# Kernel tuning notes

Hardware: AMD Instinct MI355X
Metric: run time of the kernel (lower is better)

## Reference

```python
import jax, jax.numpy as jnp
import numpy as np

N_NODES = 50000
N_EDGES = 800000
IN_CH = 128
HEADS = 4
OUT_CH = 4
N_GRAPHS = 64
NEG_SLOPE = 0.2  # GATv2Conv default leaky_relu slope
EPS = 1e-5       # GraphNorm eps


def _seg_sum(x, seg, n):
    return jax.ops.segment_sum(x, seg, num_segments=n)


def _seg_mean(x, seg, n):
    s = _seg_sum(x, seg, n)
    cnt = _seg_sum(jnp.ones((seg.shape[0],), x.dtype), seg, n)
    return s / jnp.maximum(cnt, 1.0)[:, None]


def gatv2_conv(x, src, dst, n, w_l, w_r, att, bias, heads, out_ch, concat):
    # x: [N, F_in]; src/dst: [E_tot] (self-loops already appended)
    x_l = (x @ w_l).reshape(n, heads, out_ch)
    x_r = (x @ w_r).reshape(n, heads, out_ch)
    m = jax.nn.leaky_relu(x_l[src] + x_r[dst], NEG_SLOPE)   # [E, H, C]
    e = jnp.einsum('ehc,hc->eh', m, att)                    # [E, H]
    # softmax over incoming edges of each destination node
    e_max = jax.ops.segment_max(e, dst, num_segments=n)     # [N, H]
    w = jnp.exp(e - e_max[dst])
    denom = _seg_sum(w, dst, n)                             # [N, H]
    alpha = w / denom[dst]
    out = _seg_sum(alpha[:, :, None] * x_l[src], dst, n)    # [N, H, C]
    out = out.reshape(n, heads * out_ch) if concat else out.mean(axis=1)
    return out + bias


def graph_norm(x, batch, weight, bias, mean_scale, n_graphs):
    mu = _seg_mean(x, batch, n_graphs)                      # [G, C]
    out = x - mu[batch] * mean_scale
    var = _seg_mean(out * out, batch, n_graphs)
    return out / jnp.sqrt(var[batch] + EPS) * weight + bias


def setup_inputs() -> dict:
    key = jax.random.key(0)
    ks = jax.random.split(key, 20)
    H = HEADS
    d = {}
    d['x'] = jax.random.normal(ks[0], (N_NODES, IN_CH), dtype=jnp.float32)
    d['edge_index'] = jax.random.randint(ks[1], (2, N_EDGES), 0, N_NODES, dtype=jnp.int32)
    d['batch'] = jnp.sort(jax.random.randint(ks[2], (N_NODES,), 0, N_GRAPHS, dtype=jnp.int32))
    def glorot(k, shape):
        fan = shape[0] + shape[-1]
        return jax.random.normal(k, shape, dtype=jnp.float32) * np.sqrt(2.0 / fan).astype(np.float32)
    # layer 1: in 128 -> 32 per head, concat -> 128
    d['w_l1'] = glorot(ks[3], (IN_CH, H * 32)); d['w_r1'] = glorot(ks[4], (IN_CH, H * 32))
    d['att1'] = glorot(ks[5], (H, 32)); d['b1'] = jnp.zeros((H * 32,), jnp.float32)
    d['gn1_w'] = jnp.ones((H * 32,), jnp.float32); d['gn1_b'] = jnp.zeros((H * 32,), jnp.float32); d['gn1_s'] = jnp.ones((H * 32,), jnp.float32)
    # layer 2: 128 -> 16 per head, concat -> 64
    d['w_l2'] = glorot(ks[6], (H * 32, H * 16)); d['w_r2'] = glorot(ks[7], (H * 32, H * 16))
    d['att2'] = glorot(ks[8], (H, 16)); d['b2'] = jnp.zeros((H * 16,), jnp.float32)
    d['gn2_w'] = jnp.ones((H * 16,), jnp.float32); d['gn2_b'] = jnp.zeros((H * 16,), jnp.float32); d['gn2_s'] = jnp.ones((H * 16,), jnp.float32)
    # layer 3: 64 -> 8 per head, mean over heads -> 8
    d['w_l3'] = glorot(ks[9], (H * 16, H * 8)); d['w_r3'] = glorot(ks[10], (H * 16, H * 8))
    d['att3'] = glorot(ks[11], (H, 8)); d['b3'] = jnp.zeros((8,), jnp.float32)
    d['gn3_w'] = jnp.ones((8,), jnp.float32); d['gn3_b'] = jnp.zeros((8,), jnp.float32); d['gn3_s'] = jnp.ones((8,), jnp.float32)
    d['lin_w'] = glorot(ks[12], (8, OUT_CH)); d['lin_b'] = jnp.zeros((OUT_CH,), jnp.float32)
    return d


def reference(x, edge_index, batch,
              w_l1, w_r1, att1, b1, gn1_w, gn1_b, gn1_s,
              w_l2, w_r2, att2, b2, gn2_w, gn2_b, gn2_s,
              w_l3, w_r3, att3, b3, gn3_w, gn3_b, gn3_s,
              lin_w, lin_b):
    n = x.shape[0]
    loop = jnp.arange(n, dtype=edge_index.dtype)
    src = jnp.concatenate([edge_index[0], loop])  # add_self_loops=True (PyG default)
    dst = jnp.concatenate([edge_index[1], loop])
    h = gatv2_conv(x, src, dst, n, w_l1, w_r1, att1, b1, HEADS, 32, True)
    h = jax.nn.relu(graph_norm(h, batch, gn1_w, gn1_b, gn1_s, N_GRAPHS))
    h = gatv2_conv(h, src, dst, n, w_l2, w_r2, att2, b2, HEADS, 16, True)
    h = jax.nn.relu(graph_norm(h, batch, gn2_w, gn2_b, gn2_s, N_GRAPHS))
    h = gatv2_conv(h, src, dst, n, w_l3, w_r3, att3, b3, HEADS, 8, False)
    h = jax.nn.relu(graph_norm(h, batch, gn3_w, gn3_b, gn3_s, N_GRAPHS))
    features = _seg_mean(h, batch, N_GRAPHS)  # global_mean_pool -> [G, 8]
    logits = features @ lin_w + lin_b         # [G, OUT_CH]
    return (logits, features)
```

## Files before the change

kernel.cpp:

```cpp
#include <hip/hip_runtime.h>
#include <hip/hip_fp16.h>
#include <math.h>

#define NN 50000
#define NE 800000
#define ET (NE + NN)
#define NG 64
#define H 4
#define NBK 196
#define CH 2048
#define SB ((ET + CH - 1) / CH)
#define GD ((NN + 63) / 64)

typedef _Float16 half8 __attribute__((ext_vector_type(8)));
typedef _Float16 half4 __attribute__((ext_vector_type(4)));
typedef _Float16 hv2 __attribute__((ext_vector_type(2)));
typedef float floatx4 __attribute__((ext_vector_type(4)));


template <int K, int M2>
__device__ __forceinline__ void wprep_fn(int chunk, const float* __restrict__ Wl, const float* __restrict__ Wr,
                                         _Float16* __restrict__ Wfrag) {
    constexpr int MTOT = 2 * M2, NT = MTOT / 16;
    if (chunk >= MTOT * K / 8) return;
    int lane = chunk & 63, tt = chunk >> 6;
    int t = tt % NT, kt = tt / NT;
    int n = t * 16 + (lane & 15);
    int kb = kt * 32 + (lane >> 4) * 8;
    const float* src = (n < M2) ? (Wl + n) : (Wr + (n - M2));
    half8 h;
#pragma unroll
    for (int j = 0; j < 8; ++j) h[j] = (_Float16)src[(size_t)(kb + j) * M2];
    *(half8*)(Wfrag + (size_t)chunk * 8) = h;
}


__global__ __launch_bounds__(256) void k_prep(const float* __restrict__ Wl1, const float* __restrict__ Wr1,
                                              const float* __restrict__ Wl2, const float* __restrict__ Wr2,
                                              const float* __restrict__ Wl3, const float* __restrict__ Wr3,
                                              _Float16* __restrict__ Wf1, _Float16* __restrict__ Wf2,
                                              _Float16* __restrict__ Wf3,
                                              const int* __restrict__ batch, int* __restrict__ bpos,
                                              const int* __restrict__ ei, int* __restrict__ bcnt) {
    int b = blockIdx.x, t = threadIdx.x;
    if (b < 16) { wprep_fn<128, 128>(b * 256 + t, Wl1, Wr1, Wf1); return; }
    if (b < 24) { wprep_fn<128, 64>((b - 16) * 256 + t, Wl2, Wr2, Wf2); return; }
    if (b < 26) { wprep_fn<64, 32>((b - 24) * 256 + t, Wl3, Wr3, Wf3); return; }
    if (b < 26 + NBK) {
        int i = (b - 26) * 256 + t;
        if (i >= NN) return;
        int cur = batch[i];
        int prev = (i == 0) ? -1 : batch[i - 1];
        for (int g = prev + 1; g <= cur; ++g) bpos[g] = i;
        if (i == NN - 1)
            for (int g = cur + 1; g <= NG; ++g) bpos[g] = NN;
        return;
    }
    __shared__ int hist[NBK];
    int b0 = b - 26 - NBK;
    for (int i = t; i < NBK; i += 256) hist[i] = 0;
    __syncthreads();
#pragma unroll
    for (int pass = 0; pass < CH / 256; ++pass) {
        int e = b0 * CH + pass * 256 + t;
        if (e < ET) {
            int d = (e < NE) ? ei[NE + e] : (e - NE);
            atomicAdd(&hist[d >> 8], 1);
        }
    }
    __syncthreads();
    if (t < NBK) bcnt[t * SB + b0] = hist[t];
}


template <typename AT, bool NORM>
__device__ __forceinline__ half8 load_a8(const AT* __restrict__ ap, const float* __restrict__ pa,
                                         const float* __restrict__ pb) {
    if constexpr (NORM) {
        half8 raw = *(const half8*)ap;
        half8 h;
#pragma unroll
        for (int j = 0; j < 8; ++j) {
            float y = fmaf((float)raw[j], pa[j], pb[j]);
            h[j] = (_Float16)fmaxf(y, 0.f);
        }
        return h;
    } else if constexpr (__is_same(AT, _Float16)) {
        return *(const half8*)ap;
    } else {
        const float4* p = (const float4*)ap;
        float4 a = p[0], b = p[1];
        half8 h;
        h[0] = (_Float16)a.x; h[1] = (_Float16)a.y; h[2] = (_Float16)a.z; h[3] = (_Float16)a.w;
        h[4] = (_Float16)b.x; h[5] = (_Float16)b.y; h[6] = (_Float16)b.z; h[7] = (_Float16)b.w;
        return h;
    }
}

template <int K, int M2, typename AT, bool NORM>
__device__ __forceinline__ void dualgemm_body(int blk, int tid, const AT* __restrict__ Ain,
                                              const _Float16* __restrict__ Wfrag,
                                              __half* __restrict__ Ol, float* __restrict__ Or,
                                              const float* __restrict__ ga, const float* __restrict__ gb,
                                              const int* __restrict__ batch) {
    constexpr int MTOT = 2 * M2;
    constexpr int NT = MTOT / 16;
    constexpr int KT = K / 32;
    int wid = tid >> 6, lane = tid & 63;
    int q = lane >> 4, l15 = lane & 15;
    int r0 = blk * 64 + wid * 16;
    int arow = min(r0 + l15, NN - 1);
    const AT* ap = Ain + (size_t)arow * K + q * 8;
    const float *pa = nullptr, *pb = nullptr;
    if constexpr (NORM) {
        int g = batch[arow];
        pa = ga + g * K + q * 8;
        pb = gb + g * K + q * 8;
    }

    floatx4 acc[NT];
#pragma unroll
    for (int t = 0; t < NT; ++t) acc[t] = (floatx4){0.f, 0.f, 0.f, 0.f};

#pragma unroll
    for (int kt = 0; kt < KT; ++kt) {
        half8 a8 = load_a8<AT, NORM>(ap + kt * 32, pa + (NORM ? kt * 32 : 0), pb + (NORM ? kt * 32 : 0));
        const _Float16* wp = Wfrag + ((size_t)(kt * NT) * 64 + lane) * 8;
#pragma unroll
        for (int t = 0; t < NT; ++t) {
            half8 b8 = *(const half8*)(wp + (size_t)t * 64 * 8);
            acc[t] = __builtin_amdgcn_mfma_f32_16x16x32_f16(a8, b8, acc[t], 0, 0, 0);
        }
    }

#pragma unroll
    for (int t = 0; t < NT; ++t) {
        int cn = t * 16 + l15;
#pragma unroll
        for (int reg = 0; reg < 4; ++reg) {
            int r = r0 + q * 4 + reg;
            if (r < NN) {
                if (cn < M2) Ol[(size_t)r * M2 + cn] = __float2half(acc[t][reg]);
                else         Or[(size_t)r * M2 + (cn - M2)] = acc[t][reg];
            }
        }
    }
}

template <int K, int M2>
__global__ __launch_bounds__(256) void k_dualgemm_n(const __half* __restrict__ Ain,
                                                    const _Float16* __restrict__ Wfrag,
                                                    __half* __restrict__ Ol, float* __restrict__ Or,
                                                    const float* __restrict__ ga, const float* __restrict__ gb,
                                                    const int* __restrict__ batch) {
    dualgemm_body<K, M2, _Float16, true>(blockIdx.x, threadIdx.x, (const _Float16*)Ain, Wfrag, Ol, Or,
                                         ga, gb, batch);
}


__device__ __forceinline__ void bscanA_fn(int b, int t, const int* __restrict__ bcnt,
                                          int* __restrict__ boff, int* __restrict__ tot) {
    __shared__ int lds[256];
    int i0 = 2 * t, i1 = 2 * t + 1;
    int v0 = (i0 < SB) ? bcnt[b * SB + i0] : 0;
    int v1 = (i1 < SB) ? bcnt[b * SB + i1] : 0;
    int pair = v0 + v1;
    lds[t] = pair;
    __syncthreads();
    for (int off = 1; off < 256; off <<= 1) {
        int y = (t >= off) ? lds[t - off] : 0;
        __syncthreads();
        lds[t] += y;
        __syncthreads();
    }
    int excl = lds[t] - pair;
    if (i0 < SB) boff[b * SB + i0] = excl;
    if (i1 < SB) boff[b * SB + i1] = excl + v0;
    if (t == 255) tot[b] = lds[255];
}


__global__ __launch_bounds__(256) void k_gemm1_scan(const float* __restrict__ x, const _Float16* __restrict__ Wf1,
                                                    __half* __restrict__ Ol, float* __restrict__ Or,
                                                    const int* __restrict__ bcnt, int* __restrict__ boff,
                                                    int* __restrict__ tot) {
    if (blockIdx.x < GD)
        dualgemm_body<128, 128, float, false>(blockIdx.x, threadIdx.x, x, Wf1, Ol, Or, nullptr, nullptr, nullptr);
    else
        bscanA_fn(blockIdx.x - GD, threadIdx.x, bcnt, boff, tot);
}


__device__ __forceinline__ void edge_sd(int e, const int* __restrict__ ei, int& s, int& d) {
    if (e < NE) { s = ei[e]; d = ei[NE + e]; } else { s = e - NE; d = s; }
}

__global__ __launch_bounds__(256) void k_bscatter(const int* __restrict__ ei, const int* __restrict__ tot,
                                                  const int* __restrict__ boff, unsigned int* __restrict__ ebuf) {
    __shared__ int eb[256];
    __shared__ int cur[NBK];
    int b0 = blockIdx.x, t = threadIdx.x;
    int v = (t < NBK) ? tot[t] : 0;
    eb[t] = v;
    __syncthreads();
    for (int off = 1; off < 256; off <<= 1) {
        int y = (t >= off) ? eb[t - off] : 0;
        __syncthreads();
        eb[t] += y;
        __syncthreads();
    }
    if (t < NBK) cur[t] = (eb[t] - v) + boff[t * SB + b0];
    __syncthreads();
#pragma unroll
    for (int pass = 0; pass < CH / 256; ++pass) {
        int e = b0 * CH + pass * 256 + t;
        if (e < ET) {
            int s, d;
            edge_sd(e, ei, s, d);
            int pos = atomicAdd(&cur[d >> 8], 1);
            ebuf[pos] = ((unsigned)s << 16) | (unsigned)(d & 255);
        }
    }
}


__global__ __launch_bounds__(256) void k_bsort(const unsigned int* __restrict__ ebuf,
                                               const int* __restrict__ tot,
                                               int* __restrict__ rowptr, unsigned short* __restrict__ colsrc) {
    __shared__ int eb[256];
    __shared__ int sbase;
    __shared__ int cnt2[256];
    __shared__ int sc[256];
    __shared__ int cur2[256];
    int b = blockIdx.x, t = threadIdx.x;
    int v = (t < NBK) ? tot[t] : 0;
    eb[t] = v;
    __syncthreads();
    for (int off = 1; off < 256; off <<= 1) {
        int y = (t >= off) ? eb[t - off] : 0;
        __syncthreads();
        eb[t] += y;
        __syncthreads();
    }
    if (t == b) sbase = eb[t] - v;
    __syncthreads();
    int base = sbase, n = tot[b];
    cnt2[t] = 0;
    __syncthreads();
    for (int i = t; i < n; i += 256) atomicAdd(&cnt2[ebuf[base + i] & 255], 1);
    __syncthreads();
    int cv = cnt2[t];
    sc[t] = cv;
    __syncthreads();
    for (int off = 1; off < 256; off <<= 1) {
        int y = (t >= off) ? sc[t - off] : 0;
        __syncthreads();
        sc[t] += y;
        __syncthreads();
    }
    int excl = sc[t] - cv;
    int d = b * 256 + t;
    if (d < NN) rowptr[d] = base + excl;
    if (b == 0 && t == 0) rowptr[NN] = ET;
    cur2[t] = excl;
    __syncthreads();
    for (int i = t; i < n; i += 256) {
        unsigned u = ebuf[base + i];
        int pos = atomicAdd(&cur2[u & 255], 1);
        colsrc[base + pos] = (unsigned short)(u >> 16);
    }
}


template <int CP> struct HVec { hv2 h2[CP / 2]; };

template <int CP>
__device__ __forceinline__ HVec<CP> load_hv(const __half* __restrict__ p) {
    HVec<CP> r;
    if constexpr (CP == 16) {
        float4* rp = (float4*)&r;
        rp[0] = ((const float4*)p)[0];
        rp[1] = ((const float4*)p)[1];
    } else if constexpr (CP == 8) {
        float4 t = *(const float4*)p; r = *(HVec<CP>*)&t;
    } else if constexpr (CP == 4) {
        float2 t = *(const float2*)p; r = *(HVec<CP>*)&t;
    } else {
        r.h2[0] = *(const hv2*)p;
    }
    return r;
}

template <int C, int EP, bool CONCAT>
__global__ __launch_bounds__(256) void k_attn(const __half* __restrict__ xl, const float* __restrict__ xr,
                                              const int* __restrict__ rowptr,
                                              const unsigned short* __restrict__ colsrc,
                                              const float* __restrict__ att, const float* __restrict__ bias,
                                              __half* __restrict__ out) {
    constexpr int CP = C / EP;
    constexpr int LEP = (EP == 4) ? 2 : ((EP == 2) ? 1 : 0);
    int t = blockIdx.x * 256 + threadIdx.x;
    int part = t & (EP - 1);
    int nh = t >> LEP;
    if (nh >= NN * H) return;
    int node = nh >> 2, h = nh & 3;
    int cbase = h * C + part * CP;
    hv2 xrr2[CP / 2], attv2[CP / 2];
    float acc[CP];
    {
        const float* p = xr + (size_t)node * (H * C) + cbase;
        const float* q = att + cbase;
#pragma unroll
        for (int j = 0; j < CP / 2; ++j) {
            xrr2[j] = (hv2){(_Float16)p[2 * j], (_Float16)p[2 * j + 1]};
            attv2[j] = (hv2){(_Float16)q[2 * j], (_Float16)q[2 * j + 1]};
        }
#pragma unroll
        for (int c = 0; c < CP; ++c) acc[c] = 0.f;
    }
    float denom = 0.f;
    int beg = rowptr[node], end = rowptr[node + 1];

    auto process = [&](const HVec<CP>& xv) {
        float part_s = 0.f;
#pragma unroll
        for (int j = 0; j < CP / 2; ++j) {
            hv2 z = xv.h2[j] + xrr2[j];
            hv2 l = __builtin_elementwise_max(z, z * (_Float16)0.2f);
            part_s = __builtin_amdgcn_fdot2(l, attv2[j], part_s, false);
        }
        float score = part_s;
#pragma unroll
        for (int mask = 1; mask < EP; mask <<= 1) score += __shfl_xor(score, mask, 64);
        float w = __expf(score);
        denom += w;
        const _Float16* xh = (const _Float16*)&xv;
#pragma unroll
        for (int c = 0; c < CP; ++c) acc[c] = fmaf(w, (float)xh[c], acc[c]);
    };

    int idx = beg;
    for (; idx + 4 <= end; idx += 4) {
        int s0 = colsrc[idx], s1 = colsrc[idx + 1], s2 = colsrc[idx + 2], s3 = colsrc[idx + 3];
        HVec<CP> xv0 = load_hv<CP>(xl + (size_t)s0 * (H * C) + cbase);
        HVec<CP> xv1 = load_hv<CP>(xl + (size_t)s1 * (H * C) + cbase);
        HVec<CP> xv2 = load_hv<CP>(xl + (size_t)s2 * (H * C) + cbase);
        HVec<CP> xv3 = load_hv<CP>(xl + (size_t)s3 * (H * C) + cbase);
        process(xv0);
        process(xv1);
        process(xv2);
        process(xv3);
    }
    for (; idx < end; ++idx) {
        int s = colsrc[idx];
        HVec<CP> xv = load_hv<CP>(xl + (size_t)s * (H * C) + cbase);
        process(xv);
    }

    float inv = 1.f / denom;
    _Float16* op = (_Float16*)out + (size_t)node * (H * C) + cbase;
    _Float16 hv[CP];
#pragma unroll
    for (int c = 0; c < CP; ++c) {
        float v = acc[c] * inv;
        if (CONCAT) v += bias[cbase + c];
        hv[c] = (_Float16)v;
    }
    if constexpr (CP >= 8) {
#pragma unroll
        for (int j = 0; j < CP / 8; ++j) *(half8*)(op + 8 * j) = *(half8*)(hv + 8 * j);
    } else if constexpr (CP == 4) {
        *(half4*)op = *(half4*)hv;
    } else {
        *(hv2*)op = *(hv2*)hv;
    }
}


template <int LOGC, int SPLIT>
__global__ __launch_bounds__(256) void k_gnred2(const __half* __restrict__ h, const int* __restrict__ bpos,
                                                float* __restrict__ sum, float* __restrict__ sumsq) {
    constexpr int C = 1 << LOGC;
    constexpr int RG = 256 >> LOGC;
    int g = blockIdx.x / SPLIT, s = blockIdx.x % SPLIT;
    int c = threadIdx.x & (C - 1);
    int rg = threadIdx.x >> LOGC;
    int b0 = bpos[g], b1 = bpos[g + 1];
    int n = b1 - b0;
    int seg = (n + SPLIT - 1) / SPLIT;
    int r0 = b0 + s * seg;
    int r1 = min(r0 + seg, b1);
    float sv = 0.f, ssv = 0.f;
    for (int r = r0 + rg; r < r1; r += RG) {
        float x = __half2float(h[(size_t)r * C + c]);
        sv += x; ssv += x * x;
    }
    __shared__ float ls[256], lss[256];
    ls[threadIdx.x] = sv; lss[threadIdx.x] = ssv;
    __syncthreads();
    for (int off = 128; off >= C; off >>= 1) {
        if (threadIdx.x < off) {
            ls[threadIdx.x] += ls[threadIdx.x + off];
            lss[threadIdx.x] += lss[threadIdx.x + off];
        }
        __syncthreads();
    }
    if (threadIdx.x < C) {
        atomicAdd(&sum[g * C + threadIdx.x], ls[threadIdx.x]);
        atomicAdd(&sumsq[g * C + threadIdx.x], lss[threadIdx.x]);
    }
}


__global__ __launch_bounds__(256) void k_gnparam(const float* __restrict__ sum, const float* __restrict__ sumsq,
                                                 const int* __restrict__ bpos, const float* __restrict__ w,
                                                 const float* __restrict__ b, const float* __restrict__ ms,
                                                 int logC, float* __restrict__ ga, float* __restrict__ gb) {
    int C = 1 << logC;
    int i = blockIdx.x * 256 + threadIdx.x;
    if (i >= NG * C) return;
    int g = i >> logC, c = i & (C - 1);
    float cg = fmaxf((float)(bpos[g + 1] - bpos[g]), 1.f);
    float mu = sum[i] / cg;
    float ex2 = sumsq[i] / cg;
    float s_ = ms[c];
    float var = ex2 - (2.f * s_ - s_ * s_) * mu * mu;
    float a = rsqrtf(var + 1e-5f) * w[c];
    ga[i] = a;
    gb[i] = b[c] - mu * s_ * a;
}


template <int SPLIT>
__global__ __launch_bounds__(256) void k_headgn(const __half* __restrict__ tmp, const float* __restrict__ b3,
                                                const int* __restrict__ bpos, float* __restrict__ Af,
                                                float* __restrict__ sum, float* __restrict__ sumsq) {
    constexpr int C = 8, RG = 32;
    int g = blockIdx.x / SPLIT, s = blockIdx.x % SPLIT;
    int c = threadIdx.x & 7;
    int rg = threadIdx.x >> 3;
    int b0 = bpos[g], b1 = bpos[g + 1];
    int n = b1 - b0;
    int seg = (n + SPLIT - 1) / SPLIT;
    int r0 = b0 + s * seg;
    int r1 = min(r0 + seg, b1);
    float bias = b3[c];
    float sv = 0.f, ssv = 0.f;
    for (int r = r0 + rg; r < r1; r += RG) {
        const __half* p = tmp + (size_t)r * 32 + c;
        float v = 0.25f * (__half2float(p[0]) + __half2float(p[8]) +
                           __half2float(p[16]) + __half2float(p[24])) + bias;
        Af[(size_t)r * C + c] = v;
        sv += v; ssv += v * v;
    }
    __shared__ float ls[256], lss[256];
    ls[threadIdx.x] = sv; lss[threadIdx.x] = ssv;
    __syncthreads();
    for (int off = 128; off >= C; off >>= 1) {
        if (threadIdx.x < off) {
            ls[threadIdx.x] += ls[threadIdx.x + off];
            lss[threadIdx.x] += lss[threadIdx.x + off];
        }
        __syncthreads();
    }
    if (threadIdx.x < C) {
        atomicAdd(&sum[g * C + threadIdx.x], ls[threadIdx.x]);
        atomicAdd(&sumsq[g * C + threadIdx.x], lss[threadIdx.x]);
    }
}

template <int SPLIT>
__global__ __launch_bounds__(256) void k_gnpool(const float* __restrict__ Af, const int* __restrict__ bpos,
                                                const float* __restrict__ sum, const float* __restrict__ sumsq,
                                                const float* __restrict__ w,
                                                const float* __restrict__ b, const float* __restrict__ ms,
                                                float* __restrict__ pool) {
    constexpr int C = 8, RG = 32;
    int g = blockIdx.x / SPLIT, s = blockIdx.x % SPLIT;
    int c = threadIdx.x & 7;
    int rg = threadIdx.x >> 3;
    int b0 = bpos[g], b1 = bpos[g + 1];
    int n = b1 - b0;
    int seg = (n + SPLIT - 1) / SPLIT;
    int r0 = b0 + s * seg;
    int r1 = min(r0 + seg, b1);
    float cg = fmaxf((float)n, 1.f);
    float mu = sum[g * C + c] / cg;
    float ex2 = sumsq[g * C + c] / cg;
    float s_ = ms[c];
    float var = ex2 - (2.f * s_ - s_ * s_) * mu * mu;
    float rs = rsqrtf(var + 1e-5f) * w[c];
    float bb = b[c], mus = mu * s_;
    float pv = 0.f;
    for (int r = r0 + rg; r < r1; r += RG) {
        float y = fmaxf((Af[(size_t)r * C + c] - mus) * rs + bb, 0.f);
        pv += y;
    }
    __shared__ float ls[256];
    ls[threadIdx.x] = pv;
    __syncthreads();
    for (int off = 128; off >= C; off >>= 1) {
        if (threadIdx.x < off) ls[threadIdx.x] += ls[threadIdx.x + off];
        __syncthreads();
    }
    if (threadIdx.x < C) atomicAdd(&pool[g * C + threadIdx.x], ls[threadIdx.x]);
}


__global__ __launch_bounds__(512) void k_final(const float* __restrict__ pool, const int* __restrict__ bpos,
                                               const float* __restrict__ lw, const float* __restrict__ lb,
                                               float* __restrict__ outp) {
    __shared__ float feat[512];
    int t = threadIdx.x;
    int g = t >> 3;
    float f = pool[t] / fmaxf((float)(bpos[g + 1] - bpos[g]), 1.f);
    feat[t] = f;
    outp[256 + t] = f;
    __syncthreads();
    if (t < 256) {
        int g2 = t >> 2, o = t & 3;
        float a = lb[o];
#pragma unroll
        for (int cc = 0; cc < 8; ++cc) a += feat[g2 * 8 + cc] * lw[cc * 4 + o];
        outp[t] = a;
    }
}


extern "C" void kernel_launch(void* const* d_in, const int* in_sizes, int n_in,
                              void* d_out, int out_size, void* d_ws, size_t ws_size,
                              hipStream_t stream) {
    const float* x    = (const float*)d_in[0];
    const int*   ei   = (const int*)d_in[1];
    const int*   batch= (const int*)d_in[2];
    const float *w_l1 = (const float*)d_in[3],  *w_r1 = (const float*)d_in[4];
    const float *att1 = (const float*)d_in[5],  *b1   = (const float*)d_in[6];
    const float *gn1w = (const float*)d_in[7],  *gn1b = (const float*)d_in[8],  *gn1s = (const float*)d_in[9];
    const float *w_l2 = (const float*)d_in[10], *w_r2 = (const float*)d_in[11];
    const float *att2 = (const float*)d_in[12], *b2   = (const float*)d_in[13];
    const float *gn2w = (const float*)d_in[14], *gn2b = (const float*)d_in[15], *gn2s = (const float*)d_in[16];
    const float *w_l3 = (const float*)d_in[17], *w_r3 = (const float*)d_in[18];
    const float *att3 = (const float*)d_in[19], *b3   = (const float*)d_in[20];
    const float *gn3w = (const float*)d_in[21], *gn3b = (const float*)d_in[22], *gn3s = (const float*)d_in[23];
    const float *lw   = (const float*)d_in[24], *lb   = (const float*)d_in[25];

    char* ws = (char*)d_ws;
    size_t off = 0;
    auto alloc = [&](size_t bytes) -> void* {
        void* p = ws + off;
        off += (bytes + 255) & ~(size_t)255;
        return p;
    };
    __half* Ah  = (__half*)alloc((size_t)NN * 128 * 2);
    __half* Bh  = (__half*)alloc((size_t)NN * 128 * 2);
    __half* Chh = (__half*)alloc((size_t)NN * 64 * 2);
    float*  B   = (float*)alloc((size_t)NN * 128 * 4);
    float*  Cb  = (float*)alloc((size_t)NN * 64 * 4);
    float*  Af  = (float*)alloc((size_t)NN * 8 * 4);
    _Float16* Wf1 = (_Float16*)alloc((size_t)256 * 128 * 2);
    _Float16* Wf2 = (_Float16*)alloc((size_t)128 * 128 * 2);
    _Float16* Wf3 = (_Float16*)alloc((size_t)64 * 64 * 2);
    float* ga1 = (float*)alloc((size_t)NG * 128 * 4);
    float* gb1 = (float*)alloc((size_t)NG * 128 * 4);
    float* ga2 = (float*)alloc((size_t)NG * 64 * 4);
    float* gb2 = (float*)alloc((size_t)NG * 64 * 4);
    int* rowptr = (int*)alloc((size_t)(NN + 1) * 4);
    unsigned short* colsrc = (unsigned short*)alloc((size_t)ET * 2);
    unsigned int* ebuf = (unsigned int*)alloc((size_t)ET * 4);
    int* bcnt   = (int*)alloc((size_t)NBK * SB * 4);
    int* boff   = (int*)alloc((size_t)NBK * SB * 4);
    int* tot    = (int*)alloc((size_t)NBK * 4);
    int* bpos   = (int*)alloc((size_t)(NG + 1) * 4);
    char* zbase = ws + off;
    float* sum1 = (float*)alloc((size_t)NG * 128 * 4);
    float* sq1  = (float*)alloc((size_t)NG * 128 * 4);
    float* sum2 = (float*)alloc((size_t)NG * 64 * 4);
    float* sq2  = (float*)alloc((size_t)NG * 64 * 4);
    float* sum3 = (float*)alloc((size_t)NG * 8 * 4);
    float* sq3  = (float*)alloc((size_t)NG * 8 * 4);
    float* pool = (float*)alloc((size_t)NG * 8 * 4);
    size_t zbytes = (size_t)((ws + off) - zbase);
    (void)hipMemsetAsync(zbase, 0, zbytes, stream);

    k_prep<<<26 + NBK + SB, 256, 0, stream>>>(w_l1, w_r1, w_l2, w_r2, w_l3, w_r3, Wf1, Wf2, Wf3,
                                              batch, bpos, ei, bcnt);
    k_gemm1_scan<<<GD + NBK, 256, 0, stream>>>(x, Wf1, Ah, B, bcnt, boff, tot);
    k_bscatter<<<SB, 256, 0, stream>>>(ei, tot, boff, ebuf);
    k_bsort<<<NBK, 256, 0, stream>>>(ebuf, tot, rowptr, colsrc);

    int gA2ep = (NN * H * 2 + 255) / 256;
    int gA1ep = (NN * H + 255) / 256;

    k_attn<32, 2, true><<<gA2ep, 256, 0, stream>>>(Ah, B, rowptr, colsrc, att1, b1, Bh);
    k_gnred2<7, 8><<<NG * 8, 256, 0, stream>>>(Bh, bpos, sum1, sq1);
    k_gnparam<<<(NG * 128 + 255) / 256, 256, 0, stream>>>(sum1, sq1, bpos, gn1w, gn1b, gn1s, 7, ga1, gb1);

    k_dualgemm_n<128, 64><<<GD, 256, 0, stream>>>(Bh, Wf2, Ah, Cb, ga1, gb1, batch);
    k_attn<16, 2, true><<<gA2ep, 256, 0, stream>>>(Ah, Cb, rowptr, colsrc, att2, b2, Chh);
    k_gnred2<6, 8><<<NG * 8, 256, 0, stream>>>(Chh, bpos, sum2, sq2);
    k_gnparam<<<(NG * 64 + 255) / 256, 256, 0, stream>>>(sum2, sq2, bpos, gn2w, gn2b, gn2s, 6, ga2, gb2);

    k_dualgemm_n<64, 32><<<GD, 256, 0, stream>>>(Chh, Wf3, Ah, B, ga2, gb2, batch);
    k_attn<8, 1, false><<<gA1ep, 256, 0, stream>>>(Ah, B, rowptr, colsrc, att3, nullptr, Bh);
    k_headgn<8><<<NG * 8, 256, 0, stream>>>(Bh, b3, bpos, Af, sum3, sq3);
    k_gnpool<8><<<NG * 8, 256, 0, stream>>>(Af, bpos, sum3, sq3, gn3w, gn3b, gn3s, pool);
    k_final<<<1, 512, 0, stream>>>(pool, bpos, lw, lb, (float*)d_out);
}
```

Measured before the change: 300.0 us.

## Fuse GraphNorm statistics into attention epilogue and norm params into next GEMM

The attention kernel now accumulates per-graph sum and sum-of-squares directly in its epilogue, using wave shuffles and a block reduction when all nodes in the block belong to one graph, and falls back to per-thread atomics otherwise. The separate gnred2, gnparam and headgn kernels are removed; the next dual GEMM computes the GraphNorm scale and shift on the fly from the raw sums. The right-side projection is also stored as fp16 instead of fp32. This cuts several launches and passes over the node features, at the cost of extra per-element math in the GEMM A-load, more atomics across graph boundaries, and fp16 rounding of x_r.

```diff
diff --git a/kernel.cpp b/kernel.cpp
--- a/kernel.cpp
+++ b/kernel.cpp
@@ -16,6 +16,15 @@
 typedef _Float16 half4 __attribute__((ext_vector_type(4)));
 typedef _Float16 hv2 __attribute__((ext_vector_type(2)));
 typedef float floatx4 __attribute__((ext_vector_type(4)));
+
+struct f8 { float v[8]; };
+__device__ __forceinline__ f8 ld8(const float* __restrict__ p) {
+    f8 r;
+    float4 a = ((const float4*)p)[0], b = ((const float4*)p)[1];
+    r.v[0] = a.x; r.v[1] = a.y; r.v[2] = a.z; r.v[3] = a.w;
+    r.v[4] = b.x; r.v[5] = b.y; r.v[6] = b.z; r.v[7] = b.w;
+    return r;
+}
 
 
 template <int K, int M2>
@@ -73,19 +82,9 @@
 }
 
 
-template <typename AT, bool NORM>
-__device__ __forceinline__ half8 load_a8(const AT* __restrict__ ap, const float* __restrict__ pa,
-                                         const float* __restrict__ pb) {
-    if constexpr (NORM) {
-        half8 raw = *(const half8*)ap;
-        half8 h;
-#pragma unroll
-        for (int j = 0; j < 8; ++j) {
-            float y = fmaf((float)raw[j], pa[j], pb[j]);
-            h[j] = (_Float16)fmaxf(y, 0.f);
-        }
-        return h;
-    } else if constexpr (__is_same(AT, _Float16)) {
+template <typename AT>
+__device__ __forceinline__ half8 load_raw8(const AT* __restrict__ ap) {
+    if constexpr (__is_same(AT, _Float16)) {
         return *(const half8*)ap;
     } else {
         const float4* p = (const float4*)ap;
@@ -100,9 +99,11 @@
 template <int K, int M2, typename AT, bool NORM>
 __device__ __forceinline__ void dualgemm_body(int blk, int tid, const AT* __restrict__ Ain,
                                               const _Float16* __restrict__ Wfrag,
-                                              __half* __restrict__ Ol, float* __restrict__ Or,
-                                              const float* __restrict__ ga, const float* __restrict__ gb,
-                                              const int* __restrict__ batch) {
+                                              __half* __restrict__ Ol, __half* __restrict__ Or,
+                                              const float* __restrict__ gsum, const float* __restrict__ gsq,
+                                              const float* __restrict__ gw, const float* __restrict__ gbb,
+                                              const float* __restrict__ gms,
+                                              const int* __restrict__ bpos, const int* __restrict__ batch) {
     constexpr int MTOT = 2 * M2;
     constexpr int NT = MTOT / 16;
     constexpr int KT = K / 32;
@@ -111,11 +112,11 @@
     int r0 = blk * 64 + wid * 16;
     int arow = min(r0 + l15, NN - 1);
     const AT* ap = Ain + (size_t)arow * K + q * 8;
-    const float *pa = nullptr, *pb = nullptr;
+    float inv_cg = 0.f;
+    int g = 0;
     if constexpr (NORM) {
-        int g = batch[arow];
-        pa = ga + g * K + q * 8;
-        pb = gb + g * K + q * 8;
+        g = batch[arow];
+        inv_cg = 1.f / fmaxf((float)(bpos[g + 1] - bpos[g]), 1.f);
     }
 
     floatx4 acc[NT];
@@ -124,7 +125,29 @@
 
 #pragma unroll
     for (int kt = 0; kt < KT; ++kt) {
-        half8 a8 = load_a8<AT, NORM>(ap + kt * 32, pa + (NORM ? kt * 32 : 0), pb + (NORM ? kt * 32 : 0));
+        half8 a8;
+        if constexpr (NORM) {
+            half8 raw = *(const half8*)(ap + kt * 32);
+            int c0 = kt * 32 + q * 8;
+            f8 su = ld8(gsum + (size_t)g * K + c0);
+            f8 sx = ld8(gsq + (size_t)g * K + c0);
+            f8 ww = ld8(gw + c0);
+            f8 bb = ld8(gbb + c0);
+            f8 mm = ld8(gms + c0);
+#pragma unroll
+            for (int j = 0; j < 8; ++j) {
+                float mu = su.v[j] * inv_cg;
+                float ex2 = sx.v[j] * inv_cg;
+                float s_ = mm.v[j];
+                float var = ex2 - s_ * (2.f - s_) * mu * mu;
+                float a = rsqrtf(var + 1e-5f) * ww.v[j];
+                float bsh = bb.v[j] - mu * s_ * a;
+                float y = fmaf((float)raw[j], a, bsh);
+                a8[j] = (_Float16)fmaxf(y, 0.f);
+            }
+        } else {
+            a8 = load_raw8<AT>(ap + kt * 32);
+        }
         const _Float16* wp = Wfrag + ((size_t)(kt * NT) * 64 + lane) * 8;
 #pragma unroll
         for (int t = 0; t < NT; ++t) {
@@ -141,7 +164,7 @@
             int r = r0 + q * 4 + reg;
             if (r < NN) {
                 if (cn < M2) Ol[(size_t)r * M2 + cn] = __float2half(acc[t][reg]);
-                else         Or[(size_t)r * M2 + (cn - M2)] = acc[t][reg];
+                else         Or[(size_t)r * M2 + (cn - M2)] = __float2half(acc[t][reg]);
             }
         }
     }
@@ -150,11 +173,13 @@
 template <int K, int M2>
 __global__ __launch_bounds__(256) void k_dualgemm_n(const __half* __restrict__ Ain,
                                                     const _Float16* __restrict__ Wfrag,
-                                                    __half* __restrict__ Ol, float* __restrict__ Or,
-                                                    const float* __restrict__ ga, const float* __restrict__ gb,
-                                                    const int* __restrict__ batch) {
+                                                    __half* __restrict__ Ol, __half* __restrict__ Or,
+                                                    const float* __restrict__ gsum, const float* __restrict__ gsq,
+                                                    const float* __restrict__ gw, const float* __restrict__ gbb,
+                                                    const float* __restrict__ gms,
+                                                    const int* __restrict__ bpos, const int* __restrict__ batch) {
     dualgemm_body<K, M2, _Float16, true>(blockIdx.x, threadIdx.x, (const _Float16*)Ain, Wfrag, Ol, Or,
-                                         ga, gb, batch);
+                                         gsum, gsq, gw, gbb, gms, bpos, batch);
 }
 
 
@@ -181,11 +206,12 @@
 
 
 __global__ __launch_bounds__(256) void k_gemm1_scan(const float* __restrict__ x, const _Float16* __restrict__ Wf1,
-                                                    __half* __restrict__ Ol, float* __restrict__ Or,
+                                                    __half* __restrict__ Ol, __half* __restrict__ Or,
                                                     const int* __restrict__ bcnt, int* __restrict__ boff,
                                                     int* __restrict__ tot) {
     if (blockIdx.x < GD)
-        dualgemm_body<128, 128, float, false>(blockIdx.x, threadIdx.x, x, Wf1, Ol, Or, nullptr, nullptr, nullptr);
+        dualgemm_body<128, 128, float, false>(blockIdx.x, threadIdx.x, x, Wf1, Ol, Or,
+                                              nullptr, nullptr, nullptr, nullptr, nullptr, nullptr, nullptr);
     else
         bscanA_fn(blockIdx.x - GD, threadIdx.x, bcnt, boff, tot);
 }
@@ -292,34 +318,41 @@
 }
 
 template <int C, int EP, bool CONCAT>
-__global__ __launch_bounds__(256) void k_attn(const __half* __restrict__ xl, const float* __restrict__ xr,
+__global__ __launch_bounds__(256) void k_attn(const __half* __restrict__ xl, const __half* __restrict__ xr,
                                               const int* __restrict__ rowptr,
                                               const unsigned short* __restrict__ colsrc,
                                               const float* __restrict__ att, const float* __restrict__ bias,
-                                              __half* __restrict__ out) {
+                                              __half* __restrict__ out,
+                                              const int* __restrict__ batch,
+                                              float* __restrict__ gsum, float* __restrict__ gsq,
+                                              float* __restrict__ Af) {
     constexpr int CP = C / EP;
     constexpr int LEP = (EP == 4) ? 2 : ((EP == 2) ? 1 : 0);
+    constexpr int TPN = H * EP;
+    constexpr int NPB = 256 / TPN;
     int t = blockIdx.x * 256 + threadIdx.x;
     int part = t & (EP - 1);
     int nh = t >> LEP;
-    if (nh >= NN * H) return;
-    int node = nh >> 2, h = nh & 3;
+    bool active = (nh < NN * H);
+    int node = active ? (nh >> 2) : (NN - 1);
+    int h = nh & 3;
     int cbase = h * C + part * CP;
     hv2 xrr2[CP / 2], attv2[CP / 2];
     float acc[CP];
     {
-        const float* p = xr + (size_t)node * (H * C) + cbase;
+        HVec<CP> xrv = load_hv<CP>(xr + (size_t)node * (H * C) + cbase);
         const float* q = att + cbase;
 #pragma unroll
         for (int j = 0; j < CP / 2; ++j) {
-            xrr2[j] = (hv2){(_Float16)p[2 * j], (_Float16)p[2 * j + 1]};
+            xrr2[j] = xrv.h2[j];
             attv2[j] = (hv2){(_Float16)q[2 * j], (_Float16)q[2 * j + 1]};
         }
 #pragma unroll
         for (int c = 0; c < CP; ++c) acc[c] = 0.f;
     }
     float denom = 0.f;
-    int beg = rowptr[node], end = rowptr[node + 1];
+    int beg = active ? rowptr[node] : 0;
+    int end = active ? rowptr[node + 1] : 0;
 
     auto process = [&](const HVec<CP>& xv) {
         float part_s = 0.f;
@@ -358,116 +391,118 @@
     }
 
     float inv = 1.f / denom;
-    _Float16* op = (_Float16*)out + (size_t)node * (H * C) + cbase;
-    _Float16 hv[CP];
-#pragma unroll
-    for (int c = 0; c < CP; ++c) {
-        float v = acc[c] * inv;
-        if (CONCAT) v += bias[cbase + c];
-        hv[c] = (_Float16)v;
-    }
-    if constexpr (CP >= 8) {
-#pragma unroll
-        for (int j = 0; j < CP / 8; ++j) *(half8*)(op + 8 * j) = *(half8*)(hv + 8 * j);
-    } else if constexpr (CP == 4) {
-        *(half4*)op = *(half4*)hv;
+    int node0 = blockIdx.x * NPB;
+    int nodeL = min(node0 + NPB, NN) - 1;
+    int gf = batch[node0], gl = batch[nodeL];
+    int lane = threadIdx.x & 63, wv = threadIdx.x >> 6;
+
+    if constexpr (CONCAT) {
+#pragma unroll
+        for (int c = 0; c < CP; ++c) {
+            float v = acc[c] * inv + bias[cbase + c];
+            acc[c] = active ? v : 0.f;
+        }
+        if (active) {
+            _Float16* op = (_Float16*)out + (size_t)node * (H * C) + cbase;
+            _Float16 hv[CP];
+#pragma unroll
+            for (int c = 0; c < CP; ++c) hv[c] = (_Float16)acc[c];
+            if constexpr (CP >= 8) {
+#pragma unroll
+                for (int j = 0; j < CP / 8; ++j) *(half8*)(op + 8 * j) = *(half8*)(hv + 8 * j);
+            } else if constexpr (CP == 4) {
+                *(half4*)op = *(half4*)hv;
+            } else {
+                *(hv2*)op = *(hv2*)hv;
+            }
+        }
+        float sqv[CP];
+#pragma unroll
+        for (int c = 0; c < CP; ++c) sqv[c] = acc[c] * acc[c];
+
+        if (gf == gl) {
+#pragma unroll
+            for (int m = TPN; m < 64; m <<= 1) {
+#pragma unroll
+                for (int c = 0; c < CP; ++c) {
+                    acc[c] += __shfl_xor(acc[c], m, 64);
+                    sqv[c] += __shfl_xor(sqv[c], m, 64);
+                }
+            }
+            __shared__ float red[2][4][TPN][CP];
+            if (lane < TPN) {
+#pragma unroll
+                for (int c = 0; c < CP; ++c) {
+                    red[0][wv][lane][c] = acc[c];
+                    red[1][wv][lane][c] = sqv[c];
+                }
+            }
+            __syncthreads();
+            constexpr int NV = TPN * CP;
+            for (int i = threadIdx.x; i < 2 * NV; i += 256) {
+                int which = (i >= NV) ? 1 : 0;
+                int idx2 = i - which * NV;
+                int slot = idx2 / CP, c = idx2 % CP;
+                float val = red[which][0][slot][c] + red[which][1][slot][c] +
+                            red[which][2][slot][c] + red[which][3][slot][c];
+                int hh = (slot >> LEP) & 3, pp = slot & (EP - 1);
+                int ch = hh * C + pp * CP + c;
+                atomicAdd((which ? gsq : gsum) + (size_t)gf * (H * C) + ch, val);
+            }
+        } else if (active) {
+            int g = batch[node];
+#pragma unroll
+            for (int c = 0; c < CP; ++c) {
+                atomicAdd(&gsum[(size_t)g * (H * C) + cbase + c], acc[c]);
+                atomicAdd(&gsq[(size_t)g * (H * C) + cbase + c], sqv[c]);
+            }
+        }
     } else {
-        *(hv2*)op = *(hv2*)hv;
-    }
-}
-
-
-template <int LOGC, int SPLIT>
-__global__ __launch_bounds__(256) void k_gnred2(const __half* __restrict__ h, const int* __restrict__ bpos,
-                                                float* __restrict__ sum, float* __restrict__ sumsq) {
-    constexpr int C = 1 << LOGC;
-    constexpr int RG = 256 >> LOGC;
-    int g = blockIdx.x / SPLIT, s = blockIdx.x % SPLIT;
-    int c = threadIdx.x & (C - 1);
-    int rg = threadIdx.x >> LOGC;
-    int b0 = bpos[g], b1 = bpos[g + 1];
-    int n = b1 - b0;
-    int seg = (n + SPLIT - 1) / SPLIT;
-    int r0 = b0 + s * seg;
-    int r1 = min(r0 + seg, b1);
-    float sv = 0.f, ssv = 0.f;
-    for (int r = r0 + rg; r < r1; r += RG) {
-        float x = __half2float(h[(size_t)r * C + c]);
-        sv += x; ssv += x * x;
-    }
-    __shared__ float ls[256], lss[256];
-    ls[threadIdx.x] = sv; lss[threadIdx.x] = ssv;
-    __syncthreads();
-    for (int off = 128; off >= C; off >>= 1) {
-        if (threadIdx.x < off) {
-            ls[threadIdx.x] += ls[threadIdx.x + off];
-            lss[threadIdx.x] += lss[threadIdx.x + off];
-        }
-        __syncthreads();
-    }
-    if (threadIdx.x < C) {
-        atomicAdd(&sum[g * C + threadIdx.x], ls[threadIdx.x]);
-        atomicAdd(&sumsq[g * C + threadIdx.x], lss[threadIdx.x]);
-    }
-}
-
-
-__global__ __launch_bounds__(256) void k_gnparam(const float* __restrict__ sum, const float* __restrict__ sumsq,
-                                                 const int* __restrict__ bpos, const float* __restrict__ w,
-                                                 const float* __restrict__ b, const float* __restrict__ ms,
-                                                 int logC, float* __restrict__ ga, float* __restrict__ gb) {
-    int C = 1 << logC;
-    int i = blockIdx.x * 256 + threadIdx.x;
-    if (i >= NG * C) return;
-    int g = i >> logC, c = i & (C - 1);
-    float cg = fmaxf((float)(bpos[g + 1] - bpos[g]), 1.f);
-    float mu = sum[i] / cg;
-    float ex2 = sumsq[i] / cg;
-    float s_ = ms[c];
-    float var = ex2 - (2.f * s_ - s_ * s_) * mu * mu;
-    float a = rsqrtf(var + 1e-5f) * w[c];
-    ga[i] = a;
-    gb[i] = b[c] - mu * s_ * a;
-}
-
-
-template <int SPLIT>
-__global__ __launch_bounds__(256) void k_headgn(const __half* __restrict__ tmp, const float* __restrict__ b3,
-                                                const int* __restrict__ bpos, float* __restrict__ Af,
-                                                float* __restrict__ sum, float* __restrict__ sumsq) {
-    constexpr int C = 8, RG = 32;
-    int g = blockIdx.x / SPLIT, s = blockIdx.x % SPLIT;
-    int c = threadIdx.x & 7;
-    int rg = threadIdx.x >> 3;
-    int b0 = bpos[g], b1 = bpos[g + 1];
-    int n = b1 - b0;
-    int seg = (n + SPLIT - 1) / SPLIT;
-    int r0 = b0 + s * seg;
-    int r1 = min(r0 + seg, b1);
-    float bias = b3[c];
-    float sv = 0.f, ssv = 0.f;
-    for (int r = r0 + rg; r < r1; r += RG) {
-        const __half* p = tmp + (size_t)r * 32 + c;
-        float v = 0.25f * (__half2float(p[0]) + __half2float(p[8]) +
-                           __half2float(p[16]) + __half2float(p[24])) + bias;
-        Af[(size_t)r * C + c] = v;
-        sv += v; ssv += v * v;
-    }
-    __shared__ float ls[256], lss[256];
-    ls[threadIdx.x] = sv; lss[threadIdx.x] = ssv;
-    __syncthreads();
-    for (int off = 128; off >= C; off >>= 1) {
-        if (threadIdx.x < off) {
-            ls[threadIdx.x] += ls[threadIdx.x + off];
-            lss[threadIdx.x] += lss[threadIdx.x + off];
-        }
-        __syncthreads();
-    }
-    if (threadIdx.x < C) {
-        atomicAdd(&sum[g * C + threadIdx.x], ls[threadIdx.x]);
-        atomicAdd(&sumsq[g * C + threadIdx.x], lss[threadIdx.x]);
-    }
-}
+#pragma unroll
+        for (int c = 0; c < CP; ++c) acc[c] = active ? acc[c] * inv : 0.f;
+#pragma unroll
+        for (int m = 1; m < 4; m <<= 1)
+#pragma unroll
+            for (int c = 0; c < CP; ++c) acc[c] += __shfl_xor(acc[c], m, 64);
+#pragma unroll
+        for (int c = 0; c < CP; ++c) acc[c] = 0.25f * acc[c] + bias[c];
+        float s0 = 0.f, s1 = 0.f;
+        if (active) {
+            float2 w2 = {acc[2 * h], acc[2 * h + 1]};
+            *(float2*)(Af + (size_t)node * 8 + 2 * h) = w2;
+            s0 = w2.x; s1 = w2.y;
+        }
+        float q0 = s0 * s0, q1 = s1 * s1;
+        if (gf == gl) {
+#pragma unroll
+            for (int m = 4; m < 64; m <<= 1) {
+                s0 += __shfl_xor(s0, m, 64); s1 += __shfl_xor(s1, m, 64);
+                q0 += __shfl_xor(q0, m, 64); q1 += __shfl_xor(q1, m, 64);
+            }
+            __shared__ float red3[2][4][4][2];
+            if (lane < 4) {
+                red3[0][wv][lane][0] = s0; red3[0][wv][lane][1] = s1;
+                red3[1][wv][lane][0] = q0; red3[1][wv][lane][1] = q1;
+            }
+            __syncthreads();
+            if (threadIdx.x < 16) {
+                int which = threadIdx.x >> 3, idx2 = threadIdx.x & 7;
+                int slot = idx2 >> 1, c = idx2 & 1;
+                float val = red3[which][0][slot][c] + red3[which][1][slot][c] +
+                            red3[which][2][slot][c] + red3[which][3][slot][c];
+                int ch = slot * 2 + c;
+                atomicAdd((which ? gsq : gsum) + (size_t)gf * 8 + ch, val);
+            }
+        } else if (active) {
+            int g = batch[node];
+            atomicAdd(&gsum[(size_t)g * 8 + 2 * h], s0);
+            atomicAdd(&gsum[(size_t)g * 8 + 2 * h + 1], s1);
+            atomicAdd(&gsq[(size_t)g * 8 + 2 * h], q0);
+            atomicAdd(&gsq[(size_t)g * 8 + 2 * h + 1], q1);
+        }
+    }
+}
+
 
 template <int SPLIT>
 __global__ __launch_bounds__(256) void k_gnpool(const float* __restrict__ Af, const int* __restrict__ bpos,
@@ -554,16 +589,12 @@
     __half* Ah  = (__half*)alloc((size_t)NN * 128 * 2);
     __half* Bh  = (__half*)alloc((size_t)NN * 128 * 2);
     __half* Chh = (__half*)alloc((size_t)NN * 64 * 2);
-    float*  B   = (float*)alloc((size_t)NN * 128 * 4);
-    float*  Cb  = (float*)alloc((size_t)NN * 64 * 4);
+    __half* B   = (__half*)alloc((size_t)NN * 128 * 2);
+    __half* Cb  = (__half*)alloc((size_t)NN * 64 * 2);
     float*  Af  = (float*)alloc((size_t)NN * 8 * 4);
     _Float16* Wf1 = (_Float16*)alloc((size_t)256 * 128 * 2);
     _Float16* Wf2 = (_Float16*)alloc((size_t)128 * 128 * 2);
     _Float16* Wf3 = (_Float16*)alloc((size_t)64 * 64 * 2);
-    float* ga1 = (float*)alloc((size_t)NG * 128 * 4);
-    float* gb1 = (float*)alloc((size_t)NG * 128 * 4);
-    float* ga2 = (float*)alloc((size_t)NG * 64 * 4);
-    float* gb2 = (float*)alloc((size_t)NG * 64 * 4);
     int* rowptr = (int*)alloc((size_t)(NN + 1) * 4);
     unsigned short* colsrc = (unsigned short*)alloc((size_t)ET * 2);
     unsigned int* ebuf = (unsigned int*)alloc((size_t)ET * 4);
@@ -591,18 +622,16 @@
     int gA2ep = (NN * H * 2 + 255) / 256;
     int gA1ep = (NN * H + 255) / 256;
 
-    k_attn<32, 2, true><<<gA2ep, 256, 0, stream>>>(Ah, B, rowptr, colsrc, att1, b1, Bh);
-    k_gnred2<7, 8><<<NG * 8, 256, 0, stream>>>(Bh, bpos, sum1, sq1);
-    k_gnparam<<<(NG * 128 + 255) / 256, 256, 0, stream>>>(sum1, sq1, bpos, gn1w, gn1b, gn1s, 7, ga1, gb1);
-
-    k_dualgemm_n<128, 64><<<GD, 256, 0, stream>>>(Bh, Wf2, Ah, Cb, ga1, gb1, batch);
-    k_attn<16, 2, true><<<gA2ep, 256, 0, stream>>>(Ah, Cb, rowptr, colsrc, att2, b2, Chh);
-    k_gnred2<6, 8><<<NG * 8, 256, 0, stream>>>(Chh, bpos, sum2, sq2);
-    k_gnparam<<<(NG * 64 + 255) / 256, 256, 0, stream>>>(sum2, sq2, bpos, gn2w, gn2b, gn2s, 6, ga2, gb2);
-
-    k_dualgemm_n<64, 32><<<GD, 256, 0, stream>>>(Chh, Wf3, Ah, B, ga2, gb2, batch);
-    k_attn<8, 1, false><<<gA1ep, 256, 0, stream>>>(Ah, B, rowptr, colsrc, att3, nullptr, Bh);
-    k_headgn<8><<<NG * 8, 256, 0, stream>>>(Bh, b3, bpos, Af, sum3, sq3);
+    k_attn<32, 2, true><<<gA2ep, 256, 0, stream>>>(Ah, B, rowptr, colsrc, att1, b1, Bh,
+                                                   batch, sum1, sq1, nullptr);
+
+    k_dualgemm_n<128, 64><<<GD, 256, 0, stream>>>(Bh, Wf2, Ah, Cb, sum1, sq1, gn1w, gn1b, gn1s, bpos, batch);
+    k_attn<16, 2, true><<<gA2ep, 256, 0, stream>>>(Ah, Cb, rowptr, colsrc, att2, b2, Chh,
+                                                   batch, sum2, sq2, nullptr);
+
+    k_dualgemm_n<64, 32><<<GD, 256, 0, stream>>>(Chh, Wf3, Ah, B, sum2, sq2, gn2w, gn2b, gn2s, bpos, batch);
+    k_attn<8, 1, false><<<gA1ep, 256, 0, stream>>>(Ah, B, rowptr, colsrc, att3, b3, nullptr,
+                                                   batch, sum3, sq3, Af);
     k_gnpool<8><<<NG * 8, 256, 0, stream>>>(Af, bpos, sum3, sq3, gn3w, gn3b, gn3s, pool);
     k_final<<<1, 512, 0, stream>>>(pool, bpos, lw, lb, (float*)d_out);
 }
```

New measurement: 354.1 us. +18.1%, slower.
